# Optimization experiments

Hardware: AMD Instinct MI355X
Metric: run time of the kernel (lower is better)

Reference implementation:

```python
import jax, jax.numpy as jnp
import numpy as np

B, A, G, C = 64, 8732, 50, 81
NEG_POS_RATIO = 3


def _make_boxes(key, b, n):
    k1, k2 = jax.random.split(key)
    mins = jax.random.uniform(k1, (b, n, 2)) * 0.7
    sizes = jax.random.uniform(k2, (b, n, 2)) * 0.3 + 0.01
    return jnp.concatenate([mins, mins + sizes], axis=-1)  # [b,n,4] xyxy


def setup_inputs() -> dict:
    key = jax.random.key(0)
    k1, k2, k3, k4 = jax.random.split(key, 4)
    pred_boxes = _make_boxes(k1, B, A)
    gt_boxes = _make_boxes(k2, B, G)
    pred_scores = jax.random.normal(k3, (B, A, C), dtype=jnp.float32)
    gt_labels = jax.random.randint(k4, (B, G), 0, C)
    return {"pred_boxes": pred_boxes, "pred_scores": pred_scores,
            "gt_boxes": gt_boxes, "gt_labels": gt_labels}


def _iou(a, b):
    # a: [B,A,4], b: [B,G,4] -> [B,A,G]
    a_ = a[:, :, None, :]
    b_ = b[:, None, :, :]
    iw = jnp.clip(jnp.minimum(a_[..., 2], b_[..., 2]) - jnp.maximum(a_[..., 0], b_[..., 0]), 0)
    ih = jnp.clip(jnp.minimum(a_[..., 3], b_[..., 3]) - jnp.maximum(a_[..., 1], b_[..., 1]), 0)
    inter = iw * ih
    area_a = (a_[..., 2] - a_[..., 0]) * (a_[..., 3] - a_[..., 1])
    area_b = (b_[..., 2] - b_[..., 0]) * (b_[..., 3] - b_[..., 1])
    union = jnp.clip(area_a + area_b - inter, 1e-6)
    return inter / union


def reference(pred_boxes, pred_scores, gt_boxes, gt_labels):
    num_anchors = pred_boxes.shape[1]
    iou = _iou(pred_boxes, gt_boxes)              # [B,A,G]
    best_iou = iou.max(axis=2)                    # [B,A]
    best_idx = iou.argmax(axis=2)                 # [B,A]
    pos = best_iou > 0.5

    matched_boxes = jnp.take_along_axis(gt_boxes, best_idx[..., None], axis=1)   # [B,A,4]
    matched_labels = jnp.take_along_axis(gt_labels, best_idx, axis=1)            # [B,A]
    target_boxes = jnp.where(pos[..., None], matched_boxes, 0.0)
    target_labels = jnp.where(pos, matched_labels, 0)

    pos_mask = target_labels > 0
    num_pos = pos_mask.sum(axis=1)                # [B]

    # smooth L1 (beta=1), summed over box coords
    d = pred_boxes - target_boxes
    ad = jnp.abs(d)
    sl1 = jnp.where(ad < 1.0, 0.5 * d * d, ad - 0.5).sum(axis=2)  # [B,A]
    loc_loss = (sl1 * pos_mask).sum()

    # cross entropy per anchor
    log_p = jax.nn.log_softmax(pred_scores, axis=-1)
    conf = -jnp.take_along_axis(log_p, target_labels[..., None], axis=-1)[..., 0]  # [B,A]

    conf_pos = (conf * pos_mask).sum()

    # hard negative mining: top (3*num_pos) losses among negatives
    conf_neg = jnp.where(pos_mask, -1.0, conf)
    num_neg = jnp.minimum(NEG_POS_RATIO * num_pos, num_anchors - 1)   # [B]
    order = jnp.argsort(-conf_neg, axis=1)        # descending
    rank = jnp.argsort(order, axis=1)             # rank of each anchor in sorted order
    hard_neg = rank < num_neg[:, None]
    conf_neg_hard = (conf * hard_neg).sum()

    total = (loc_loss + conf_pos + conf_neg_hard) / jnp.maximum(num_pos, 1).sum()
    return total
```

## Files before the change

### kernel.cpp

```cpp
#include <hip/hip_runtime.h>

#define BB 64
#define AA 8732
#define GG 50
#define CC 81
#define NEG_RATIO 3
#define HW 16
#define HSTRIDE 257
#define NCHUNK 137
#define XB 16


__device__ __forceinline__ unsigned mono_key(float f) {
    unsigned u = __float_as_uint(f);
    u = (u & 0x80000000u) ? ~u : (u | 0x80000000u);
    return ~u;
}

__device__ __forceinline__ float unkey_val(unsigned key) {
    unsigned u = ~key;
    return __uint_as_float((u & 0x80000000u) ? (u & 0x7fffffffu) : ~u);
}

__global__ __launch_bounds__(256, 4) void k_match(
    const float* __restrict__ pred_boxes, const float* __restrict__ pred_scores,
    const float* __restrict__ gt_boxes, const int* __restrict__ gt_labels,
    float* __restrict__ confneg_out,
    float* __restrict__ acc_slots, int* __restrict__ np_slots,
    unsigned* __restrict__ ctr)
{
    __shared__ float4 sgt[GG];
    __shared__ float  sarea[GG];
    __shared__ int    slab[GG];
    __shared__ float  redf[4];
    __shared__ int    redi[4];

    const int tid = threadIdx.x;
    const int b = blockIdx.y;
    const int x = blockIdx.x;
    const int grp = tid >> 2;
    const int q   = tid & 3;

    if (b == 0 && x == 0 && tid == 0) *ctr = 0u;

    if (tid < GG) {
        float4 g4 = ((const float4*)gt_boxes)[b * GG + tid];
        sgt[tid] = g4;
        sarea[tid] = (g4.z - g4.x) * (g4.w - g4.y);
        slab[tid] = gt_labels[b * GG + tid];
    }
    __syncthreads();

    const float*  sb = pred_scores + (size_t)b * AA * CC;
    const float4* bbx = (const float4*)pred_boxes + (size_t)b * AA;

    float contrib = 0.f;
    int npos = 0;

    int a0 = x * 64 + grp;
    int am = a0 < AA ? a0 : AA - 1;
    float4 nbox = bbx[am];
    const float* nrow = sb + (size_t)am * CC;
    float4 ns0 = *(const float4*)(nrow + 4 * q);
    float4 ns1 = *(const float4*)(nrow + 4 * q + 16);
    float4 ns2 = *(const float4*)(nrow + 4 * q + 32);
    float4 ns3 = *(const float4*)(nrow + 4 * q + 48);
    float4 ns4 = *(const float4*)(nrow + 4 * q + 64);
    float  ns80 = nrow[80];

    for (int c = x; c < NCHUNK; c += XB) {
        const float4 pb = nbox;
        const float4 s0 = ns0, s1 = ns1, s2 = ns2, s3 = ns3, s4 = ns4;
        const float  s80 = ns80;
        const float* crow = nrow;
        const int a = c * 64 + grp;
        const bool valid = a < AA;

        int cnx = c + XB; if (cnx >= NCHUNK) cnx = c;
        int an = cnx * 64 + grp; if (an >= AA) an = AA - 1;
        nbox = bbx[an];
        nrow = sb + (size_t)an * CC;
        ns0 = *(const float4*)(nrow + 4 * q);
        ns1 = *(const float4*)(nrow + 4 * q + 16);
        ns2 = *(const float4*)(nrow + 4 * q + 32);
        ns3 = *(const float4*)(nrow + 4 * q + 48);
        ns4 = *(const float4*)(nrow + 4 * q + 64);
        ns80 = nrow[80];

        const float area_p = (pb.z - pb.x) * (pb.w - pb.y);
        float best = -1.f; int bidx = 0x7fffffff;
        #pragma unroll
        for (int i = 0; i < 13; ++i) {
            const int g = q + (i << 2);
            const bool gv = g < GG;
            const int gc = gv ? g : 0;
            const float4 gb = sgt[gc];
            const float  sa = sarea[gc];
            float iw = fmaxf(fminf(pb.z, gb.z) - fmaxf(pb.x, gb.x), 0.f);
            float ih = fmaxf(fminf(pb.w, gb.w) - fmaxf(pb.y, gb.y), 0.f);
            float inter = iw * ih;
            float uni = fmaxf(area_p + sa - inter, 1e-6f);
            float iou = __fdividef(inter, uni);
            if (gv && iou > best) { best = iou; bidx = g; }
        }
        #pragma unroll
        for (int off = 1; off < 4; off <<= 1) {
            float ov = __shfl_xor(best, off);
            int   oi = __shfl_xor(bidx, off);
            if (ov > best || (ov == best && oi < bidx)) { best = ov; bidx = oi; }
        }
        const int label = (best > 0.5f) ? slab[bidx] : 0;

        float sm = 0.f;
        sm += __expf(s0.x) + __expf(s0.y) + __expf(s0.z) + __expf(s0.w);
        sm += __expf(s1.x) + __expf(s1.y) + __expf(s1.z) + __expf(s1.w);
        sm += __expf(s2.x) + __expf(s2.y) + __expf(s2.z) + __expf(s2.w);
        sm += __expf(s3.x) + __expf(s3.y) + __expf(s3.z) + __expf(s3.w);
        sm += __expf(s4.x) + __expf(s4.y) + __expf(s4.z) + __expf(s4.w);
        if (q == 0) sm += __expf(s80);
        sm += __shfl_xor(sm, 1);
        sm += __shfl_xor(sm, 2);

        if (q == 0 && valid) {
            const float labv = crow[label];
            const float conf = __logf(sm) - labv;
            const size_t ai = (size_t)b * AA + a;
            const bool pm = label > 0;
            confneg_out[ai] = pm ? -1.f : conf;
            if (pm) {
                npos++;
                const float4 gb = sgt[bidx];
                float sl1 = 0.f, d, ad;
                d = pb.x - gb.x; ad = fabsf(d); sl1 += (ad < 1.f) ? 0.5f * d * d : ad - 0.5f;
                d = pb.y - gb.y; ad = fabsf(d); sl1 += (ad < 1.f) ? 0.5f * d * d : ad - 0.5f;
                d = pb.z - gb.z; ad = fabsf(d); sl1 += (ad < 1.f) ? 0.5f * d * d : ad - 0.5f;
                d = pb.w - gb.w; ad = fabsf(d); sl1 += (ad < 1.f) ? 0.5f * d * d : ad - 0.5f;
                contrib += sl1 + conf;
            }
        }
    }

    #pragma unroll
    for (int off = 32; off; off >>= 1) {
        contrib += __shfl_down(contrib, off);
        npos    += __shfl_down(npos, off);
    }
    const int wv = tid >> 6;
    if ((tid & 63) == 0) { redf[wv] = contrib; redi[wv] = npos; }
    __syncthreads();
    if (tid == 0) {
        acc_slots[b * XB + x] = redf[0] + redf[1] + redf[2] + redf[3];
        np_slots[b * XB + x]  = redi[0] + redi[1] + redi[2] + redi[3];
    }
}

__global__ __launch_bounds__(1024) void k_hardneg(
    const float* __restrict__ confneg,
    const int* __restrict__ np_slots, const float* __restrict__ acc_slots,
    float* __restrict__ per_b, int* __restrict__ den_b,
    unsigned* __restrict__ ctr, float* __restrict__ out)
{
    __shared__ unsigned hist[HW * HSTRIDE];
    __shared__ unsigned binsum[256];
    __shared__ unsigned sel[2];
    __shared__ unsigned uE[HW], uG[HW], eb[HW];
    __shared__ float    fred[HW];
    __shared__ int      stot;
    __shared__ int      slast;

    const int b = blockIdx.x;
    const int tid = threadIdx.x;
    const int wv = tid >> 6;
    const int lane = tid & 63;

    int np = 0;
    #pragma unroll
    for (int i = 0; i < XB; ++i) np += np_slots[b * XB + i];
    int k = NEG_RATIO * np; if (k > AA - 1) k = AA - 1;

    float hn = 0.f;
    if (k > 0) {
        const float* cn = confneg + (size_t)b * AA;

        const int lo = tid * 9;
        int nk = AA - lo; nk = nk > 9 ? 9 : (nk < 0 ? 0 : nk);
        unsigned keys[9];
        #pragma unroll
        for (int j = 0; j < 9; ++j)
            if (j < nk) keys[j] = mono_key(cn[lo + j]);

        unsigned prefix = 0, kk = (unsigned)k;
        for (int lev = 0; lev < 4; ++lev) {
            const int shift = 24 - 8 * lev;
            for (int i = tid; i < HW * HSTRIDE; i += 1024) hist[i] = 0;
            __syncthreads();
            #pragma unroll
            for (int j = 0; j < 9; ++j) {
                if (j < nk) {
                    const unsigned key = keys[j];
                    if (lev == 0 || (key >> (shift + 8)) == prefix)
                        atomicAdd(&hist[wv * HSTRIDE + ((key >> shift) & 255u)], 1u);
                }
            }
            __syncthreads();
            if (tid < 256) {
                unsigned s = 0;
                #pragma unroll
                for (int w = 0; w < HW; ++w) s += hist[w * HSTRIDE + tid];
                binsum[tid] = s;
            }
            __syncthreads();
            if (wv == 0) {
                const unsigned v0 = binsum[4 * lane], v1 = binsum[4 * lane + 1];
                const unsigned v2 = binsum[4 * lane + 2], v3 = binsum[4 * lane + 3];
                const unsigned lsum = v0 + v1 + v2 + v3;
                unsigned sc = lsum;
                #pragma unroll
                for (int off = 1; off < 64; off <<= 1) {
                    unsigned t = __shfl_up(sc, off);
                    if (lane >= off) sc += t;
                }
                const unsigned excl = sc - lsum;
                if (kk > excl && kk <= sc) {
                    unsigned cacc = excl;
                    if (kk <= cacc + v0)              { sel[0] = 4 * lane;     sel[1] = kk - cacc; }
                    else if (kk <= (cacc += v0) + v1) { sel[0] = 4 * lane + 1; sel[1] = kk - cacc; }
                    else if (kk <= (cacc += v1) + v2) { sel[0] = 4 * lane + 2; sel[1] = kk - cacc; }
                    else                              { sel[0] = 4 * lane + 3; sel[1] = kk - cacc - v2; }
                }
            }
            __syncthreads();
            prefix = (prefix << 8) | sel[0];
            kk = sel[1];
        }
        const unsigned kth = prefix;

        int cntG = 0, cntE = 0; float sum_gt = 0.f;
        #pragma unroll
        for (int j = 0; j < 9; ++j) {
            if (j < nk) {
                if (keys[j] < kth)       { cntG++; sum_gt += unkey_val(keys[j]); }
                else if (keys[j] == kth) { cntE++; }
            }
        }
        int sc = cntE;
        #pragma unroll
        for (int off = 1; off < 64; off <<= 1) {
            int t = __shfl_up(sc, off);
            if (lane >= off) sc += t;
        }
        int gt = cntG;
        #pragma unroll
        for (int off = 32; off; off >>= 1) gt += __shfl_down(gt, off);
        if (lane == 63) uE[wv] = (unsigned)sc;
        if (lane == 0)  uG[wv] = (unsigned)gt;
        __syncthreads();
        if (wv == 0) {
            unsigned e = (lane < HW) ? uE[lane] : 0u;
            unsigned g = (lane < HW) ? uG[lane] : 0u;
            unsigned se = e;
            #pragma unroll
            for (int off = 1; off < 16; off <<= 1) {
                unsigned t = __shfl_up(se, off);
                if (lane >= off) se += t;
            }
            if (lane < HW) eb[lane] = se - e;
            #pragma unroll
            for (int off = 8; off; off >>= 1) g += __shfl_down(g, off);
            if (lane == 0) stot = (int)g;
        }
        __syncthreads();
        const int m = k - stot;
        const int exclE = (int)eb[wv] + (sc - cntE);

        float sum_eq = 0.f;
        if (m > 0 && cntE > 0) {
            int seen = 0;
            #pragma unroll
            for (int j = 0; j < 9; ++j) {
                if (j < nk && keys[j] == kth) {
                    if (exclE + seen < m) sum_eq += unkey_val(keys[j]);
                    seen++;
                }
            }
        }

        float contrib = sum_gt + sum_eq;
        #pragma unroll
        for (int off = 32; off; off >>= 1) contrib += __shfl_down(contrib, off);
        if (lane == 0) fred[wv] = contrib;
        __syncthreads();
        if (tid == 0) {
            #pragma unroll
            for (int w = 0; w < HW; ++w) hn += fred[w];
        }
    }

    if (tid == 0) {
        float accb = 0.f;
        #pragma unroll
        for (int i = 0; i < XB; ++i) accb += acc_slots[b * XB + i];
        atomicExch(&per_b[b], accb + hn);
        atomicExch(&den_b[b], np > 1 ? np : 1);
        __threadfence();
        unsigned prev = atomicAdd(ctr, 1u);
        slast = (prev == (unsigned)(BB - 1)) ? 1 : 0;
    }
    __syncthreads();
    if (slast && tid < BB) {
        float v = atomicAdd(&per_b[tid], 0.f);
        int   d = atomicAdd(&den_b[tid], 0);
        #pragma unroll
        for (int off = 32; off; off >>= 1) {
            v += __shfl_down(v, off);
            d += __shfl_down(d, off);
        }
        if (tid == 0) out[0] = v / (float)d;
    }
}

extern "C" void kernel_launch(void* const* d_in, const int* in_sizes, int n_in,
                              void* d_out, int out_size, void* d_ws, size_t ws_size,
                              hipStream_t stream) {
    const float* pred_boxes  = (const float*)d_in[0];
    const float* pred_scores = (const float*)d_in[1];
    const float* gt_boxes    = (const float*)d_in[2];
    const int*   gt_labels   = (const int*)d_in[3];

    float*    ws        = (float*)d_ws;
    float*    acc_slots = ws;
    int*      np_slots  = (int*)(ws + 1024);
    float*    per_b     = ws + 2048;
    int*      den_b     = (int*)(ws + 2112);
    unsigned* ctr       = (unsigned*)(ws + 2176);
    float*    conf_neg  = ws + 4096;

    dim3 g1(XB, BB);
    k_match<<<g1, 256, 0, stream>>>(pred_boxes, pred_scores, gt_boxes, gt_labels,
                                    conf_neg, acc_slots, np_slots, ctr);
    k_hardneg<<<BB, 1024, 0, stream>>>(conf_neg, np_slots, acc_slots,
                                       per_b, den_b, ctr, (float*)d_out);
}
```

Measured before the change: 300.7 us.

## Prefetch next chunk's exp sum and raise match grid to 27 blocks per batch

The match kernel now computes the softmax partial exp-sum for the next anchor chunk right after loading it, so only the partial sum is carried across iterations instead of the full score vectors. This cuts live registers, and the launch bound is raised to 5 blocks per CU to match. The grid per batch grows from 16 to 27 blocks, which spreads the 137 chunks more evenly and raises parallelism, and the workspace offsets are enlarged to hold the extra slots. The label-score load is issued before the shuffle reduction, and the first-iteration guard for out-of-range anchors is dropped because every start chunk is in range.

```diff
diff --git a/kernel.cpp b/kernel.cpp
--- a/kernel.cpp
+++ b/kernel.cpp
@@ -8,7 +8,7 @@
 #define HW 16
 #define HSTRIDE 257
 #define NCHUNK 137
-#define XB 16
+#define XB 27
 
 
 __device__ __forceinline__ unsigned mono_key(float f) {
@@ -22,7 +22,7 @@
     return __uint_as_float((u & 0x80000000u) ? (u & 0x7fffffffu) : ~u);
 }
 
-__global__ __launch_bounds__(256, 4) void k_match(
+__global__ __launch_bounds__(256, 5) void k_match(
     const float* __restrict__ pred_boxes, const float* __restrict__ pred_scores,
     const float* __restrict__ gt_boxes, const int* __restrict__ gt_labels,
     float* __restrict__ confneg_out,
@@ -57,36 +57,43 @@
     float contrib = 0.f;
     int npos = 0;
 
-    int a0 = x * 64 + grp;
-    int am = a0 < AA ? a0 : AA - 1;
-    float4 nbox = bbx[am];
-    const float* nrow = sb + (size_t)am * CC;
-    float4 ns0 = *(const float4*)(nrow + 4 * q);
-    float4 ns1 = *(const float4*)(nrow + 4 * q + 16);
-    float4 ns2 = *(const float4*)(nrow + 4 * q + 32);
-    float4 ns3 = *(const float4*)(nrow + 4 * q + 48);
-    float4 ns4 = *(const float4*)(nrow + 4 * q + 64);
-    float  ns80 = nrow[80];
+    const int a0 = x * 64 + grp;
+    float4 cbox = bbx[a0];
+    const float* crow = sb + (size_t)a0 * CC;
+    float psum;
+    {
+        const float4 v0 = *(const float4*)(crow + 4 * q);
+        const float4 v1 = *(const float4*)(crow + 4 * q + 16);
+        const float4 v2 = *(const float4*)(crow + 4 * q + 32);
+        const float4 v3 = *(const float4*)(crow + 4 * q + 48);
+        const float4 v4 = *(const float4*)(crow + 4 * q + 64);
+        const float  v80 = crow[80];
+        float ps = 0.f;
+        ps += __expf(v0.x) + __expf(v0.y) + __expf(v0.z) + __expf(v0.w);
+        ps += __expf(v1.x) + __expf(v1.y) + __expf(v1.z) + __expf(v1.w);
+        ps += __expf(v2.x) + __expf(v2.y) + __expf(v2.z) + __expf(v2.w);
+        ps += __expf(v3.x) + __expf(v3.y) + __expf(v3.z) + __expf(v3.w);
+        ps += __expf(v4.x) + __expf(v4.y) + __expf(v4.z) + __expf(v4.w);
+        if (q == 0) ps += __expf(v80);
+        psum = ps;
+    }
 
     for (int c = x; c < NCHUNK; c += XB) {
-        const float4 pb = nbox;
-        const float4 s0 = ns0, s1 = ns1, s2 = ns2, s3 = ns3, s4 = ns4;
-        const float  s80 = ns80;
-        const float* crow = nrow;
         const int a = c * 64 + grp;
         const bool valid = a < AA;
 
         int cnx = c + XB; if (cnx >= NCHUNK) cnx = c;
         int an = cnx * 64 + grp; if (an >= AA) an = AA - 1;
-        nbox = bbx[an];
-        nrow = sb + (size_t)an * CC;
-        ns0 = *(const float4*)(nrow + 4 * q);
-        ns1 = *(const float4*)(nrow + 4 * q + 16);
-        ns2 = *(const float4*)(nrow + 4 * q + 32);
-        ns3 = *(const float4*)(nrow + 4 * q + 48);
-        ns4 = *(const float4*)(nrow + 4 * q + 64);
-        ns80 = nrow[80];
-
+        const float4 nbox = bbx[an];
+        const float* nrow = sb + (size_t)an * CC;
+        const float4 n0 = *(const float4*)(nrow + 4 * q);
+        const float4 n1 = *(const float4*)(nrow + 4 * q + 16);
+        const float4 n2 = *(const float4*)(nrow + 4 * q + 32);
+        const float4 n3 = *(const float4*)(nrow + 4 * q + 48);
+        const float4 n4 = *(const float4*)(nrow + 4 * q + 64);
+        const float  n80 = nrow[80];
+
+        const float4 pb = cbox;
         const float area_p = (pb.z - pb.x) * (pb.w - pb.y);
         float best = -1.f; int bidx = 0x7fffffff;
         #pragma unroll
@@ -111,18 +118,13 @@
         }
         const int label = (best > 0.5f) ? slab[bidx] : 0;
 
-        float sm = 0.f;
-        sm += __expf(s0.x) + __expf(s0.y) + __expf(s0.z) + __expf(s0.w);
-        sm += __expf(s1.x) + __expf(s1.y) + __expf(s1.z) + __expf(s1.w);
-        sm += __expf(s2.x) + __expf(s2.y) + __expf(s2.z) + __expf(s2.w);
-        sm += __expf(s3.x) + __expf(s3.y) + __expf(s3.z) + __expf(s3.w);
-        sm += __expf(s4.x) + __expf(s4.y) + __expf(s4.z) + __expf(s4.w);
-        if (q == 0) sm += __expf(s80);
+        const float labv = crow[label];
+
+        float sm = psum;
         sm += __shfl_xor(sm, 1);
         sm += __shfl_xor(sm, 2);
 
         if (q == 0 && valid) {
-            const float labv = crow[label];
             const float conf = __logf(sm) - labv;
             const size_t ai = (size_t)b * AA + a;
             const bool pm = label > 0;
@@ -138,6 +140,16 @@
                 contrib += sl1 + conf;
             }
         }
+
+        float ps = 0.f;
+        ps += __expf(n0.x) + __expf(n0.y) + __expf(n0.z) + __expf(n0.w);
+        ps += __expf(n1.x) + __expf(n1.y) + __expf(n1.z) + __expf(n1.w);
+        ps += __expf(n2.x) + __expf(n2.y) + __expf(n2.z) + __expf(n2.w);
+        ps += __expf(n3.x) + __expf(n3.y) + __expf(n3.z) + __expf(n3.w);
+        ps += __expf(n4.x) + __expf(n4.y) + __expf(n4.z) + __expf(n4.w);
+        if (q == 0) ps += __expf(n80);
+
+        cbox = nbox; crow = nrow; psum = ps;
     }
 
     #pragma unroll
@@ -329,11 +341,11 @@
 
     float*    ws        = (float*)d_ws;
     float*    acc_slots = ws;
-    int*      np_slots  = (int*)(ws + 1024);
-    float*    per_b     = ws + 2048;
-    int*      den_b     = (int*)(ws + 2112);
-    unsigned* ctr       = (unsigned*)(ws + 2176);
-    float*    conf_neg  = ws + 4096;
+    int*      np_slots  = (int*)(ws + 2048);
+    float*    per_b     = ws + 4096;
+    int*      den_b     = (int*)(ws + 4160);
+    unsigned* ctr       = (unsigned*)(ws + 4224);
+    float*    conf_neg  = ws + 8192;
 
     dim3 g1(XB, BB);
     k_match<<<g1, 256, 0, stream>>>(pred_boxes, pred_scores, gt_boxes, gt_labels,
```

New measurement: 348.4 us. 15.8% more time.
